# Kernel optimization log

Hardware: AMD Instinct MI355X
Metric: run time of the kernel (lower is better)

Reference implementation:

```python
import jax, jax.numpy as jnp
import numpy as np

B, V, S = 16, 100000, 4096
LOSS_WEIGHT = 1.0


def setup_inputs() -> dict:
    key = jax.random.key(0)
    k1, k2, k3, k4 = jax.random.split(key, 4)
    return {
        "src_verts": jax.random.normal(k1, (B, V, 3), dtype=jnp.float32),
        "dst_verts": jax.random.normal(k2, (B, V, 3), dtype=jnp.float32),
        "src_idx": jax.random.randint(k3, (B, S), 0, V, dtype=jnp.int64),
        "dst_idx": jax.random.randint(k4, (B, S), 0, V, dtype=jnp.int64),
    }


def _gather(verts, idx):
    # verts: (B, V, 3), idx: (B, S) -> (B, S, 3)
    return jnp.take_along_axis(verts, idx[:, :, None], axis=1)


def reference(src_verts, dst_verts, src_idx, dst_idx):
    src = _gather(src_verts, src_idx)  # (B, S, 3)
    dst = _gather(dst_verts, dst_idx)  # (B, S, 3)
    # squared euclidean distance matrix, matching torch.cdist(p=2)**2
    s2 = jnp.sum(src * src, axis=-1)  # (B, S)
    d2 = jnp.sum(dst * dst, axis=-1)  # (B, S)
    gram = jnp.einsum("bsc,btc->bst", src, dst)  # (B, S, S)
    dist_mat = jnp.maximum(s2[:, :, None] + d2[:, None, :] - 2.0 * gram, 0.0)
    # min over src points (dim=1) + min over dst points (dim=2)
    chamfer_distance = jnp.min(dist_mat, axis=1) + jnp.min(dist_mat, axis=2)  # (B, S)
    chamfer_loss = jnp.mean(chamfer_distance, axis=-1)  # (B,)
    chamfer_loss = jnp.mean(chamfer_loss, axis=0)  # scalar ('mean' reduction)
    return chamfer_loss * LOSS_WEIGHT
```

## Files before the change

kernel.cpp:

```cpp
#include <hip/hip_runtime.h>
#include <hip/hip_bf16.h>
#include <math.h>

#define B 16
#define V 100000
#define S 4096
#define BS (B * S)
#define NT 256
#define ONE_BF 0x3F80u

typedef __attribute__((ext_vector_type(8))) short bf16x8;
typedef __attribute__((ext_vector_type(16))) float f32x16;

static __device__ __forceinline__ unsigned bft(float x) {
  return __float_as_uint(x) >> 16;
}
static __device__ __forceinline__ float bff(unsigned hbits) {
  return __uint_as_float(hbits << 16);
}
static __device__ __forceinline__ unsigned pk(unsigned lo, unsigned hi) {
  return (lo & 0xFFFFu) | (hi << 16);
}
static __device__ __forceinline__ float min3(float a, float b, float c) {
  return fminf(fminf(a, b), c);
}


__global__ __launch_bounds__(256) void chamfer_prep_kernel(
    const float* __restrict__ src_verts, const float* __restrict__ dst_verts,
    const int* __restrict__ src_idx, const int* __restrict__ dst_idx,
    uint4* __restrict__ srcfrag, uint4* __restrict__ dstfrag,
    float* __restrict__ out) {
  int t = blockIdx.x * 256 + threadIdx.x;
  if (t == 0) *out = 0.f;
  int set = t >> 15;
  int i0 = (t & 32767) * 2;
  int b = i0 >> 12;

  const int* idx = set ? dst_idx : src_idx;
  const float* verts = set ? dst_verts : src_verts;
  int v0 = idx[i0], v1 = idx[i0 + 1];
  v0 = v0 < 0 ? 0 : (v0 >= V ? V - 1 : v0);
  v1 = v1 < 0 ? 0 : (v1 >= V ? V - 1 : v1);
  const float* p0 = verts + ((size_t)b * V + v0) * 3;
  const float* p1 = verts + ((size_t)b * V + v1) * 3;
  float x0 = p0[0], y0 = p0[1], z0 = p0[2];
  float x1 = p1[0], y1 = p1[1], z1 = p1[2];

  #pragma unroll
  for (int k = 0; k < 2; ++k) {
    float x = k ? x1 : x0, y = k ? y1 : y0, z = k ? z1 : z0;
    int i = i0 + k;
    unsigned hx = bft(x), hy = bft(y), hz = bft(z);
    float n2 = x * x + y * y + z * z;
    unsigned n2h = bft(n2);
    unsigned n2l = bft(n2 - bff(n2h));
    if (set == 0) {
      unsigned lx = bft(x - bff(hx)), ly = bft(y - bff(hy)), lz = bft(z - bff(hz));
      int tile = i >> 5, c = i & 31;
      uint4* base = srcfrag + (size_t)tile * 64;
      base[c]      = make_uint4(pk(hx, hy), pk(hz, lx), pk(ly, lz), pk(hx, hy));
      base[32 + c] = make_uint4(pk(hz, n2h), pk(n2l, ONE_BF), pk(ONE_BF, 0u), 0u);
    } else {
      unsigned mx = bft(-2.f * bff(hx)), my = bft(-2.f * bff(hy)), mz = bft(-2.f * bff(hz));
      unsigned nx = bft(-2.f * (x - bff(hx)));
      unsigned ny = bft(-2.f * (y - bff(hy)));
      unsigned nz = bft(-2.f * (z - bff(hz)));
      dstfrag[(size_t)i * 2]     = make_uint4(pk(mx, my), pk(mz, mx), pk(my, mz), pk(nx, ny));
      dstfrag[(size_t)i * 2 + 1] = make_uint4(pk(nz, ONE_BF), pk(ONE_BF, n2h), pk(n2l, 0u), 0u);
    }
  }
}

__global__ __launch_bounds__(NT, 2) void chamfer_mfma_kernel(
    const uint4* __restrict__ srcfrag, const uint4* __restrict__ dstfrag,
    float* __restrict__ part_src, float* __restrict__ part_dst) {
  __shared__ struct {
    uint4 sfrag[2048];
    unsigned smin[1024];
  } sh;
  float* red = (float*)sh.sfrag;

  int bid = blockIdx.x;
  int b = bid >> 6;
  int jp = (bid >> 2) & 15;
  int iq = bid & 3;
  int tid = threadIdx.x;

  const uint4* chunk = srcfrag + (size_t)(b * 128 + iq * 32) * 64;
  #pragma unroll
  for (int k = 0; k < 8; ++k) {
    sh.sfrag[tid + k * NT] = chunk[tid + k * NT];
  }
  #pragma unroll
  for (int k = 0; k < 4; ++k) sh.smin[tid + k * NT] = 0x7F800000u;

  int w = tid >> 6;
  int lane = tid & 63;
  int c = lane & 31, h = lane >> 5;
  int gj = b * S + jp * 256 + w * 64 + c;
  bf16x8 A0 = __builtin_bit_cast(bf16x8, dstfrag[(size_t)gj * 2 + h]);
  bf16x8 A1 = __builtin_bit_cast(bf16x8, dstfrag[(size_t)(gj + 32) * 2 + h]);

  __syncthreads();

  f32x16 zero = {};
  f32x16 mn0, mn1;
  #pragma unroll
  for (int r = 0; r < 16; ++r) { mn0[r] = INFINITY; mn1[r] = INFINITY; }

  int t0r = 8 * w;
  #pragma unroll 4
  for (int it = 0; it < 32; ++it) {
    int t = (it + t0r) & 31;
    bf16x8 Bf = __builtin_bit_cast(bf16x8, sh.sfrag[t * 64 + lane]);
    f32x16 d0 = __builtin_amdgcn_mfma_f32_32x32x16_bf16(A0, Bf, zero, 0, 0, 0);
    f32x16 d1 = __builtin_amdgcn_mfma_f32_32x32x16_bf16(A1, Bf, zero, 0, 0, 0);
    #pragma unroll
    for (int r = 0; r < 16; ++r) mn0[r] = fminf(mn0[r], d0[r]);
    #pragma unroll
    for (int r = 0; r < 16; ++r) mn1[r] = fminf(mn1[r], d1[r]);
    float t0 = min3(d0[0], d0[1], d0[2]);
    float t1 = min3(d0[3], d0[4], d0[5]);
    float t2 = min3(d0[6], d0[7], d0[8]);
    float t3 = min3(d0[9], d0[10], d0[11]);
    float t4 = min3(d0[12], d0[13], d0[14]);
    float u0 = min3(t0, t1, t2);
    float u1 = min3(t3, t4, d0[15]);
    float s0 = min3(d1[0], d1[1], d1[2]);
    float s1 = min3(d1[3], d1[4], d1[5]);
    float s2 = min3(d1[6], d1[7], d1[8]);
    float s3 = min3(d1[9], d1[10], d1[11]);
    float s4 = min3(d1[12], d1[13], d1[14]);
    float v0 = min3(s0, s1, s2);
    float v1 = min3(s3, s4, d1[15]);
    float m = fminf(min3(u0, u1, v0), v1);
    atomicMin(&sh.smin[t * 32 + c], __float_as_uint(fmaxf(m, 0.f)));
  }

  __syncthreads();
  #pragma unroll
  for (int k = 0; k < 4; ++k) {
    int p = tid + k * NT;
    part_src[jp * BS + b * S + iq * 1024 + p] = __uint_as_float(sh.smin[p]);
  }
  __syncthreads();

  #pragma unroll
  for (int r = 0; r < 16; ++r) {
    int row = w * 64 + (r & 3) + 8 * (r >> 2) + 4 * h;
    red[row * 33 + c] = mn0[r];
    red[(row + 32) * 33 + c] = mn1[r];
  }
  __syncthreads();
  {
    int row = tid;
    const float* rp = red + row * 33;
    float a0 = min3(rp[0], rp[1], rp[2]);
    float a1 = min3(rp[3], rp[4], rp[5]);
    float a2 = min3(rp[6], rp[7], rp[8]);
    float a3 = min3(rp[9], rp[10], rp[11]);
    float a4 = min3(rp[12], rp[13], rp[14]);
    float a5 = min3(rp[15], rp[16], rp[17]);
    float a6 = min3(rp[18], rp[19], rp[20]);
    float a7 = min3(rp[21], rp[22], rp[23]);
    float a8 = min3(rp[24], rp[25], rp[26]);
    float a9 = min3(rp[27], rp[28], rp[29]);
    float aa = fminf(rp[30], rp[31]);
    float b0 = min3(a0, a1, a2);
    float b1 = min3(a3, a4, a5);
    float b2 = min3(a6, a7, a8);
    float b3 = min3(a9, aa, b0);
    float m = min3(b1, b2, b3);
    part_dst[iq * BS + b * S + jp * 256 + row] = fmaxf(m, 0.f);
  }
}

__global__ __launch_bounds__(128) void chamfer_reduce_kernel(
    const float* __restrict__ parts, float* __restrict__ out) {
  __shared__ float red[2];
  int tid = threadIdx.x;
  int i4 = blockIdx.x * 128 + tid;

  const float4* ps = (const float4*)parts;
  const float4* pd = (const float4*)(parts + 16 * BS);

  float4 ms = ps[i4];
  #pragma unroll
  for (int j = 1; j < 16; ++j) {
    float4 t = ps[j * (BS / 4) + i4];
    ms.x = fminf(ms.x, t.x); ms.y = fminf(ms.y, t.y);
    ms.z = fminf(ms.z, t.z); ms.w = fminf(ms.w, t.w);
  }
  float4 md = pd[i4];
  #pragma unroll
  for (int j = 1; j < 4; ++j) {
    float4 t = pd[j * (BS / 4) + i4];
    md.x = fminf(md.x, t.x); md.y = fminf(md.y, t.y);
    md.z = fminf(md.z, t.z); md.w = fminf(md.w, t.w);
  }
  float v = (ms.x + ms.y + ms.z + ms.w) + (md.x + md.y + md.z + md.w);
  v *= (1.0f / (float)BS);

  #pragma unroll
  for (int off = 32; off > 0; off >>= 1) v += __shfl_down(v, off, 64);
  if ((tid & 63) == 0) red[tid >> 6] = v;
  __syncthreads();
  if (tid == 0) atomicAdd(out, red[0] + red[1]);
}

extern "C" void kernel_launch(void* const* d_in, const int* in_sizes, int n_in,
                              void* d_out, int out_size, void* d_ws, size_t ws_size,
                              hipStream_t stream) {
  const float* src_verts = (const float*)d_in[0];
  const float* dst_verts = (const float*)d_in[1];
  const int* src_idx = (const int*)d_in[2];
  const int* dst_idx = (const int*)d_in[3];
  float* out = (float*)d_out;

  float* parts = (float*)d_ws;
  float* part_src = parts;
  float* part_dst = parts + 16 * BS;
  uint4* srcfrag = (uint4*)(parts + 21 * BS);
  uint4* dstfrag = (uint4*)(parts + 29 * BS);

  chamfer_prep_kernel<<<256, 256, 0, stream>>>(
      src_verts, dst_verts, src_idx, dst_idx, srcfrag, dstfrag, out);

  chamfer_mfma_kernel<<<B * 16 * 4, NT, 0, stream>>>(
      srcfrag, dstfrag, part_src, part_dst);

  chamfer_reduce_kernel<<<128, 128, 0, stream>>>(parts, out);
}
```

Before: 30.75 us.

## Compute both chamfer directions as separate symmetric passes, dropping shared atomics

```diff
diff --git a/kernel.cpp b/kernel.cpp
--- a/kernel.cpp
+++ b/kernel.cpp
@@ -29,7 +29,7 @@
 __global__ __launch_bounds__(256) void chamfer_prep_kernel(
     const float* __restrict__ src_verts, const float* __restrict__ dst_verts,
     const int* __restrict__ src_idx, const int* __restrict__ dst_idx,
-    uint4* __restrict__ srcfrag, uint4* __restrict__ dstfrag,
+    uint4* __restrict__ afrag, uint4* __restrict__ bfrag,
     float* __restrict__ out) {
   int t = blockIdx.x * 256 + threadIdx.x;
   if (t == 0) *out = 0.f;
@@ -47,60 +47,60 @@
   float x0 = p0[0], y0 = p0[1], z0 = p0[2];
   float x1 = p1[0], y1 = p1[1], z1 = p1[2];
 
+  uint4* af = afrag + (size_t)set * 2 * BS;
+  uint4* bf = bfrag + (size_t)set * 2 * BS;
+
   #pragma unroll
   for (int k = 0; k < 2; ++k) {
     float x = k ? x1 : x0, y = k ? y1 : y0, z = k ? z1 : z0;
     int i = i0 + k;
     unsigned hx = bft(x), hy = bft(y), hz = bft(z);
+    float lxf = x - bff(hx), lyf = y - bff(hy), lzf = z - bff(hz);
     float n2 = x * x + y * y + z * z;
     unsigned n2h = bft(n2);
     unsigned n2l = bft(n2 - bff(n2h));
-    if (set == 0) {
-      unsigned lx = bft(x - bff(hx)), ly = bft(y - bff(hy)), lz = bft(z - bff(hz));
-      int tile = i >> 5, c = i & 31;
-      uint4* base = srcfrag + (size_t)tile * 64;
-      base[c]      = make_uint4(pk(hx, hy), pk(hz, lx), pk(ly, lz), pk(hx, hy));
-      base[32 + c] = make_uint4(pk(hz, n2h), pk(n2l, ONE_BF), pk(ONE_BF, 0u), 0u);
-    } else {
-      unsigned mx = bft(-2.f * bff(hx)), my = bft(-2.f * bff(hy)), mz = bft(-2.f * bff(hz));
-      unsigned nx = bft(-2.f * (x - bff(hx)));
-      unsigned ny = bft(-2.f * (y - bff(hy)));
-      unsigned nz = bft(-2.f * (z - bff(hz)));
-      dstfrag[(size_t)i * 2]     = make_uint4(pk(mx, my), pk(mz, mx), pk(my, mz), pk(nx, ny));
-      dstfrag[(size_t)i * 2 + 1] = make_uint4(pk(nz, ONE_BF), pk(ONE_BF, n2h), pk(n2l, 0u), 0u);
-    }
-  }
-}
-
-__global__ __launch_bounds__(NT, 2) void chamfer_mfma_kernel(
-    const uint4* __restrict__ srcfrag, const uint4* __restrict__ dstfrag,
-    float* __restrict__ part_src, float* __restrict__ part_dst) {
-  __shared__ struct {
-    uint4 sfrag[2048];
-    unsigned smin[1024];
-  } sh;
-  float* red = (float*)sh.sfrag;
+    unsigned lx = bft(lxf), ly = bft(lyf), lz = bft(lzf);
+    int tile = i >> 5, c = i & 31;
+    bf[(size_t)tile * 64 + c]      = make_uint4(pk(hx, hy), pk(hz, lx), pk(ly, lz), pk(hx, hy));
+    bf[(size_t)tile * 64 + 32 + c] = make_uint4(pk(hz, n2h), pk(n2l, ONE_BF), pk(ONE_BF, 0u), 0u);
+    unsigned mx = bft(-2.f * bff(hx)), my = bft(-2.f * bff(hy)), mz = bft(-2.f * bff(hz));
+    unsigned nx = bft(-2.f * lxf), ny = bft(-2.f * lyf), nz = bft(-2.f * lzf);
+    af[(size_t)i * 2]     = make_uint4(pk(mx, my), pk(mz, mx), pk(my, mz), pk(nx, ny));
+    af[(size_t)i * 2 + 1] = make_uint4(pk(nz, ONE_BF), pk(ONE_BF, n2h), pk(n2l, 0u), 0u);
+  }
+}
+
+__global__ __launch_bounds__(NT, 4) void chamfer_min_kernel(
+    const uint4* __restrict__ afrag, const uint4* __restrict__ bfrag,
+    float* __restrict__ parts) {
+  __shared__ uint4 shraw[2112];
+  uint4* sfrag = shraw;
+  float* red = (float*)shraw;
 
   int bid = blockIdx.x;
-  int b = bid >> 6;
-  int jp = (bid >> 2) & 15;
-  int iq = bid & 3;
+  int dir = bid >> 10;
+  int rem = bid & 1023;
+  int b = rem >> 6;
+  int jp = (rem >> 2) & 15;
+  int iq = rem & 3;
   int tid = threadIdx.x;
 
-  const uint4* chunk = srcfrag + (size_t)(b * 128 + iq * 32) * 64;
+  int qset = dir;
+  int oset = 1 - dir;
+
+  const uint4* chunk = bfrag + (size_t)oset * 2 * BS + (size_t)(b * 128 + iq * 32) * 64;
   #pragma unroll
   for (int k = 0; k < 8; ++k) {
-    sh.sfrag[tid + k * NT] = chunk[tid + k * NT];
-  }
-  #pragma unroll
-  for (int k = 0; k < 4; ++k) sh.smin[tid + k * NT] = 0x7F800000u;
+    sfrag[tid + k * NT] = chunk[tid + k * NT];
+  }
 
   int w = tid >> 6;
   int lane = tid & 63;
   int c = lane & 31, h = lane >> 5;
   int gj = b * S + jp * 256 + w * 64 + c;
-  bf16x8 A0 = __builtin_bit_cast(bf16x8, dstfrag[(size_t)gj * 2 + h]);
-  bf16x8 A1 = __builtin_bit_cast(bf16x8, dstfrag[(size_t)(gj + 32) * 2 + h]);
+  const uint4* af = afrag + (size_t)qset * 2 * BS;
+  bf16x8 A0 = __builtin_bit_cast(bf16x8, af[(size_t)gj * 2 + h]);
+  bf16x8 A1 = __builtin_bit_cast(bf16x8, af[(size_t)(gj + 32) * 2 + h]);
 
   __syncthreads();
 
@@ -113,39 +113,16 @@
   #pragma unroll 4
   for (int it = 0; it < 32; ++it) {
     int t = (it + t0r) & 31;
-    bf16x8 Bf = __builtin_bit_cast(bf16x8, sh.sfrag[t * 64 + lane]);
+    bf16x8 Bf = __builtin_bit_cast(bf16x8, sfrag[t * 64 + lane]);
     f32x16 d0 = __builtin_amdgcn_mfma_f32_32x32x16_bf16(A0, Bf, zero, 0, 0, 0);
     f32x16 d1 = __builtin_amdgcn_mfma_f32_32x32x16_bf16(A1, Bf, zero, 0, 0, 0);
     #pragma unroll
     for (int r = 0; r < 16; ++r) mn0[r] = fminf(mn0[r], d0[r]);
     #pragma unroll
     for (int r = 0; r < 16; ++r) mn1[r] = fminf(mn1[r], d1[r]);
-    float t0 = min3(d0[0], d0[1], d0[2]);
-    float t1 = min3(d0[3], d0[4], d0[5]);
-    float t2 = min3(d0[6], d0[7], d0[8]);
-    float t3 = min3(d0[9], d0[10], d0[11]);
-    float t4 = min3(d0[12], d0[13], d0[14]);
-    float u0 = min3(t0, t1, t2);
-    float u1 = min3(t3, t4, d0[15]);
-    float s0 = min3(d1[0], d1[1], d1[2]);
-    float s1 = min3(d1[3], d1[4], d1[5]);
-    float s2 = min3(d1[6], d1[7], d1[8]);
-    float s3 = min3(d1[9], d1[10], d1[11]);
-    float s4 = min3(d1[12], d1[13], d1[14]);
-    float v0 = min3(s0, s1, s2);
-    float v1 = min3(s3, s4, d1[15]);
-    float m = fminf(min3(u0, u1, v0), v1);
-    atomicMin(&sh.smin[t * 32 + c], __float_as_uint(fmaxf(m, 0.f)));
-  }
-
-  __syncthreads();
-  #pragma unroll
-  for (int k = 0; k < 4; ++k) {
-    int p = tid + k * NT;
-    part_src[jp * BS + b * S + iq * 1024 + p] = __uint_as_float(sh.smin[p]);
-  }
-  __syncthreads();
-
+  }
+
+  __syncthreads();
   #pragma unroll
   for (int r = 0; r < 16; ++r) {
     int row = w * 64 + (r & 3) + 8 * (r >> 2) + 4 * h;
@@ -172,7 +149,7 @@
     float b2 = min3(a6, a7, a8);
     float b3 = min3(a9, aa, b0);
     float m = min3(b1, b2, b3);
-    part_dst[iq * BS + b * S + jp * 256 + row] = fmaxf(m, 0.f);
+    parts[(size_t)(dir * 4 + iq) * BS + b * S + jp * 256 + row] = fmaxf(m, 0.f);
   }
 }
 
@@ -183,11 +160,11 @@
   int i4 = blockIdx.x * 128 + tid;
 
   const float4* ps = (const float4*)parts;
-  const float4* pd = (const float4*)(parts + 16 * BS);
+  const float4* pd = (const float4*)(parts + 4 * BS);
 
   float4 ms = ps[i4];
   #pragma unroll
-  for (int j = 1; j < 16; ++j) {
+  for (int j = 1; j < 4; ++j) {
     float4 t = ps[j * (BS / 4) + i4];
     ms.x = fminf(ms.x, t.x); ms.y = fminf(ms.y, t.y);
     ms.z = fminf(ms.z, t.z); ms.w = fminf(ms.w, t.w);
@@ -219,16 +196,13 @@
   float* out = (float*)d_out;
 
   float* parts = (float*)d_ws;
-  float* part_src = parts;
-  float* part_dst = parts + 16 * BS;
-  uint4* srcfrag = (uint4*)(parts + 21 * BS);
-  uint4* dstfrag = (uint4*)(parts + 29 * BS);
+  uint4* afrag = (uint4*)d_ws + 2 * BS;
+  uint4* bfrag = (uint4*)d_ws + 6 * BS;
 
   chamfer_prep_kernel<<<256, 256, 0, stream>>>(
-      src_verts, dst_verts, src_idx, dst_idx, srcfrag, dstfrag, out);
-
-  chamfer_mfma_kernel<<<B * 16 * 4, NT, 0, stream>>>(
-      srcfrag, dstfrag, part_src, part_dst);
+      src_verts, dst_verts, src_idx, dst_idx, afrag, bfrag, out);
+
+  chamfer_min_kernel<<<2 * B * 16 * 4, NT, 0, stream>>>(afrag, bfrag, parts);
 
   chamfer_reduce_kernel<<<128, 128, 0, stream>>>(parts, out);
 }
```

Measured after the change: 36.41 us. +18.4%, slower.
